# Optimization experiments

Measured on AMD Instinct MI355X. Metric: run time of the kernel, lower is better.

Reference implementation:

```python
import jax, jax.numpy as jnp
import numpy as np

D_MODEL = 1024
N_HEADS = 16
D_HEAD = D_MODEL // N_HEADS


def setup_inputs() -> dict:
    key = jax.random.key(0)
    ks = jax.random.split(key, 9)
    s = 1.0 / np.sqrt(D_MODEL)
    x = jax.random.normal(ks[0], (2, 2048, D_MODEL), dtype=jnp.float32)
    Wq = jax.random.uniform(ks[1], (D_MODEL, D_MODEL), jnp.float32, -s, s)
    bq = jax.random.uniform(ks[2], (D_MODEL,), jnp.float32, -s, s)
    Wk = jax.random.uniform(ks[3], (D_MODEL, D_MODEL), jnp.float32, -s, s)
    bk = jax.random.uniform(ks[4], (D_MODEL,), jnp.float32, -s, s)
    Wv = jax.random.uniform(ks[5], (D_MODEL, D_MODEL), jnp.float32, -s, s)
    bv = jax.random.uniform(ks[6], (D_MODEL,), jnp.float32, -s, s)
    Wo = jax.random.uniform(ks[7], (D_MODEL, D_MODEL), jnp.float32, -s, s)
    bo = jax.random.uniform(ks[8], (D_MODEL,), jnp.float32, -s, s)
    return {"x": x, "Wq": Wq, "bq": bq, "Wk": Wk, "bk": bk,
            "Wv": Wv, "bv": bv, "Wo": Wo, "bo": bo}


def reference(x, Wq, bq, Wk, bk, Wv, bv, Wo, bo):
    B, T, _ = x.shape
    # projections: (B, T, d_model) -> (B, H, T, d_head)
    def split_heads(y):
        return y.reshape(B, T, N_HEADS, D_HEAD).transpose(0, 2, 1, 3)
    Q = split_heads(x @ Wq + bq)
    K = split_heads(x @ Wk + bk)
    V = split_heads(x @ Wv + bv)
    scores = jnp.einsum('bhqd,bhkd->bhqk', Q, K) / jnp.sqrt(jnp.float32(D_HEAD))
    causal = jnp.tril(jnp.ones((T, T), dtype=bool))  # allowed positions
    scores = jnp.where(causal, scores, -jnp.inf)
    attn = jax.nn.softmax(scores, axis=-1)
    out = jnp.einsum('bhqk,bhkd->bhqd', attn, V)
    out = out.transpose(0, 2, 1, 3).reshape(B, T, D_MODEL)
    return out @ Wo + bo
```

## Files before the change

kernel.cpp:

```cpp
#include <hip/hip_runtime.h>

typedef unsigned short u16;
typedef unsigned int u32;

#define DM 1024
#define NH 16
#define DH 64
#define BB 2
#define TT 2048

#define SCLQ 0.18033688f

using frag8  = __attribute__((ext_vector_type(8))) short;
using bf16x8 = __attribute__((ext_vector_type(8))) __bf16;
using f32x4  = __attribute__((ext_vector_type(4))) float;

__device__ inline u16 f2bf(float f) {
  union { float f; u32 u; } v; v.f = f;
  u32 r = v.u + 0x7fffu + ((v.u >> 16) & 1u);
  return (u16)(r >> 16);
}

__device__ inline f32x4 mfma_bf16(frag8 a, frag8 b, f32x4 c) {
  return __builtin_amdgcn_mfma_f32_16x16x32_bf16(
      __builtin_bit_cast(bf16x8, a), __builtin_bit_cast(bf16x8, b), c, 0, 0, 0);
}

__device__ inline void gld16(void* lds, const void* g) {
  __builtin_amdgcn_global_load_lds(
      (const __attribute__((address_space(1))) void*)g,
      (__attribute__((address_space(3))) void*)lds, 16, 0, 0);
}

__device__ inline int swi(int row, int chunk) {
  return row * 64 + ((chunk ^ (row & 7)) << 3);
}

__global__ __launch_bounds__(256) void cvt_x_kernel(const float* __restrict__ X,
                                                    u16* __restrict__ Y) {
  int i = blockIdx.x * 256 + threadIdx.x;
  float4 v = ((const float4*)X)[i];
  ushort4 o;
  o.x = f2bf(v.x); o.y = f2bf(v.y); o.z = f2bf(v.z); o.w = f2bf(v.w);
  ((ushort4*)Y)[i] = o;
}

__global__ __launch_bounds__(256) void transpose_w_kernel(
    const float* __restrict__ W0, const float* __restrict__ W1,
    const float* __restrict__ W2, const float* __restrict__ W3,
    u16* __restrict__ O0, u16* __restrict__ O1,
    u16* __restrict__ O2, u16* __restrict__ O3) {
  const float* W; u16* Ot;
  switch (blockIdx.z) {
    case 0: W = W0; Ot = O0; break;
    case 1: W = W1; Ot = O1; break;
    case 2: W = W2; Ot = O2; break;
    default: W = W3; Ot = O3; break;
  }
  __shared__ u16 Ls[64][72];
  int tid = threadIdx.x;
  int n0 = blockIdx.x * 64;
  int k0 = blockIdx.y * 64;
#pragma unroll
  for (int p = 0; p < 4; ++p) {
    int id = tid + p * 256;
    int row = id >> 4;
    int c4 = (id & 15) * 4;
    float4 v = *(const float4*)&W[(size_t)(k0 + row) * DM + n0 + c4];
    ushort4 o; o.x = f2bf(v.x); o.y = f2bf(v.y); o.z = f2bf(v.z); o.w = f2bf(v.w);
    *(ushort4*)&Ls[row][c4] = o;
  }
  __syncthreads();
#pragma unroll
  for (int p = 0; p < 4; ++p) {
    int id = tid + p * 256;
    int row = id >> 4;
    int c4 = (id & 15) * 4;
    ushort4 o;
    o.x = Ls[c4 + 0][row]; o.y = Ls[c4 + 1][row];
    o.z = Ls[c4 + 2][row]; o.w = Ls[c4 + 3][row];
    *(ushort4*)&Ot[(size_t)(n0 + row) * DM + k0 + c4] = o;
  }
}

__global__ __launch_bounds__(256, 3) void gemm_qkv_kernel(
    const u16* __restrict__ A, const u16* __restrict__ Bt,
    const float* __restrict__ b0, const float* __restrict__ b1,
    const float* __restrict__ b2,
    u16* __restrict__ QK, u16* __restrict__ Vb) {
  constexpr int K = 1024;
  __shared__ u16 As[2][4096];
  __shared__ u16 Bs[2][4096];
  int tid = threadIdx.x;
  int lane = tid & 63, w = tid >> 6;
  int qd = lane >> 4, ln = lane & 15;
  int wm = (w & 1) * 64, wn = (w >> 1) * 64;
  int m0 = blockIdx.y * 128, n0 = blockIdx.x * 128;
  f32x4 z = {0.f, 0.f, 0.f, 0.f};
  f32x4 acc[4][4];
#pragma unroll
  for (int mi = 0; mi < 4; ++mi)
#pragma unroll
    for (int ni = 0; ni < 4; ++ni) acc[mi][ni] = z;

  const u16* ga = A + (size_t)(m0 + w * 32 + (lane >> 2)) * K + (lane & 3) * 8;
  const u16* gb = Bt + (size_t)(n0 + w * 32 + (lane >> 2)) * K + (lane & 3) * 8;

  gld16(&As[0][w * 1024],       ga);
  gld16(&As[0][w * 1024 + 512], ga + 16 * K);
  gld16(&Bs[0][w * 1024],       gb);
  gld16(&Bs[0][w * 1024 + 512], gb + 16 * K);

  for (int k0 = 0; k0 < K; k0 += 32) {
    int cur = (k0 >> 5) & 1;
    __syncthreads();
    if (k0 + 32 < K) {
      int nb = cur ^ 1;
      gld16(&As[nb][w * 1024],       ga + k0 + 32);
      gld16(&As[nb][w * 1024 + 512], ga + k0 + 32 + 16 * K);
      gld16(&Bs[nb][w * 1024],       gb + k0 + 32);
      gld16(&Bs[nb][w * 1024 + 512], gb + k0 + 32 + 16 * K);
    }
    frag8 af[4], bfr[4];
#pragma unroll
    for (int mi = 0; mi < 4; ++mi)
      af[mi] = *(const frag8*)&As[cur][(wm + mi * 16 + ln) * 32 + qd * 8];
#pragma unroll
    for (int ni = 0; ni < 4; ++ni)
      bfr[ni] = *(const frag8*)&Bs[cur][(wn + ni * 16 + ln) * 32 + qd * 8];
#pragma unroll
    for (int mi = 0; mi < 4; ++mi)
#pragma unroll
      for (int ni = 0; ni < 4; ++ni)
        acc[mi][ni] = mfma_bf16(af[mi], bfr[ni], acc[mi][ni]);
  }

#pragma unroll
  for (int ni = 0; ni < 4; ++ni) {
    int col = n0 + wn + ni * 16 + ln;
    if (col < 2048) {
      bool isq = col < 1024;
      float bias = isq ? b0[col] : b1[col - 1024];
#pragma unroll
      for (int mi = 0; mi < 4; ++mi) {
        int row = m0 + wm + mi * 16 + qd * 4;
#pragma unroll
        for (int r = 0; r < 4; ++r) {
          float v = acc[mi][ni][r] + bias;
          if (isq) v *= SCLQ;
          QK[(size_t)(row + r) * 2048 + col] = f2bf(v);
        }
      }
    } else {
      int c2 = col - 2048;
      float bias = b2[c2];
#pragma unroll
      for (int mi = 0; mi < 4; ++mi) {
        int row = m0 + wm + mi * 16 + qd * 4;
#pragma unroll
        for (int r = 0; r < 4; ++r)
          Vb[(size_t)(row + r) * 1024 + c2] = f2bf(acc[mi][ni][r] + bias);
      }
    }
  }
}

__global__ __launch_bounds__(256) void gemm_out_kernel(
    const u16* __restrict__ A, const u16* __restrict__ Bt,
    const float* __restrict__ b0, float* __restrict__ Cf) {
  constexpr int K = 1024;
  __shared__ u16 As[2][4096];
  __shared__ u16 Bs[2][2048];
  int tid = threadIdx.x;
  int lane = tid & 63, w = tid >> 6;
  int qd = lane >> 4, ln = lane & 15;
  int m0 = blockIdx.y * 128, n0 = blockIdx.x * 64;
  f32x4 z = {0.f, 0.f, 0.f, 0.f};
  f32x4 acc[2][4];
#pragma unroll
  for (int mi = 0; mi < 2; ++mi)
#pragma unroll
    for (int ni = 0; ni < 4; ++ni) acc[mi][ni] = z;

  const u16* ga = A + (size_t)(m0 + w * 32 + (lane >> 2)) * K + (lane & 3) * 8;
  const u16* gb = Bt + (size_t)(n0 + w * 16 + (lane >> 2)) * K + (lane & 3) * 8;

  gld16(&As[0][w * 1024],       ga);
  gld16(&As[0][w * 1024 + 512], ga + 16 * K);
  gld16(&Bs[0][w * 512],        gb);

  for (int k0 = 0; k0 < K; k0 += 32) {
    int cur = (k0 >> 5) & 1;
    __syncthreads();
    if (k0 + 32 < K) {
      int nb = cur ^ 1;
      gld16(&As[nb][w * 1024],       ga + k0 + 32);
      gld16(&As[nb][w * 1024 + 512], ga + k0 + 32 + 16 * K);
      gld16(&Bs[nb][w * 512],        gb + k0 + 32);
    }
    frag8 af[2], bfr[4];
#pragma unroll
    for (int mi = 0; mi < 2; ++mi)
      af[mi] = *(const frag8*)&As[cur][(w * 32 + mi * 16 + ln) * 32 + qd * 8];
#pragma unroll
    for (int ni = 0; ni < 4; ++ni)
      bfr[ni] = *(const frag8*)&Bs[cur][(ni * 16 + ln) * 32 + qd * 8];
#pragma unroll
    for (int mi = 0; mi < 2; ++mi)
#pragma unroll
      for (int ni = 0; ni < 4; ++ni)
        acc[mi][ni] = mfma_bf16(af[mi], bfr[ni], acc[mi][ni]);
  }

#pragma unroll
  for (int ni = 0; ni < 4; ++ni) {
    int col = n0 + ni * 16 + ln;
    float bias = b0[col];
#pragma unroll
    for (int mi = 0; mi < 2; ++mi) {
      int row = m0 + w * 32 + mi * 16 + qd * 4;
#pragma unroll
      for (int r = 0; r < 4; ++r)
        Cf[(size_t)(row + r) * 1024 + col] = acc[mi][ni][r] + bias;
    }
  }
}

__global__ __launch_bounds__(256) void transpose_v_kernel(const u16* __restrict__ V,
                                                          u16* __restrict__ Vt) {
  int bh = blockIdx.y;
  int b = bh >> 4, h = bh & 15;
  int t0 = blockIdx.x * 64;
  __shared__ u16 Ls[64][72];
  int tid = threadIdx.x;
#pragma unroll
  for (int p = 0; p < 2; ++p) {
    int id = tid + p * 256;
    int row = id >> 3, seg = id & 7;
    *(uint4*)&Ls[row][seg * 8] =
        *(const uint4*)&V[(size_t)(b * TT + t0 + row) * DM + h * DH + seg * 8];
  }
  __syncthreads();
#pragma unroll
  for (int p = 0; p < 2; ++p) {
    int id = tid + p * 256;
    int d = id >> 3, seg = id & 7;
    union { u16 s[8]; uint4 v; } tmp;
#pragma unroll
    for (int j = 0; j < 8; ++j) tmp.s[j] = Ls[seg * 8 + j][d];
    *(uint4*)&Vt[(size_t)(bh * DH + d) * TT + t0 + seg * 8] = tmp.v;
  }
}

__global__ __launch_bounds__(256, 3) void flash4_kernel(const u16* __restrict__ QK,
                                                        const u16* __restrict__ Vt,
                                                        u16* __restrict__ O) {
  int pj = blockIdx.x;
  int bh = blockIdx.y;
  int b = bh >> 4, h = bh & 15;
  int qtA = pj, qtB = 31 - pj;
  int q0A = qtA * 64, q0B = qtB * 64;
  __shared__ u16 Ks[2 * 4096];
  __shared__ u16 Vs[2 * 4096];
  __shared__ u16 PsA[4096];
  __shared__ u16 PsB[4096];
  int tid = threadIdx.x;
  int lane = tid & 63, w = tid >> 6;
  int qd = lane >> 4, ln = lane & 15;

  frag8 qfA[2], qfB[2];
#pragma unroll
  for (int kk = 0; kk < 2; ++kk) {
    qfA[kk] = *(const frag8*)&QK[(size_t)(b * TT + q0A + w * 16 + ln) * 2048 +
                                 h * 64 + kk * 32 + qd * 8];
    qfB[kk] = *(const frag8*)&QK[(size_t)(b * TT + q0B + w * 16 + ln) * 2048 +
                                 h * 64 + kk * 32 + qd * 8];
  }

  int lr = lane >> 3, lc = (lane & 7) ^ lr;
  const u16* KgA = &QK[(size_t)(b * TT + w * 16 + lr) * 2048 + 1024 + h * 64 + lc * 8];
  const u16* KgB = KgA + 8 * 2048;
  const u16* VgA = &Vt[(size_t)(bh * 64 + w * 16 + lr) * 2048 + lc * 8];
  const u16* VgB = VgA + 8 * 2048;
  int ldsw = w * 1024;

  int nkt = qtB + 1;

  gld16(&Ks[ldsw],       KgA);
  gld16(&Ks[ldsw + 512], KgB);
  gld16(&Vs[ldsw],       VgA);
  gld16(&Vs[ldsw + 512], VgB);

  float lA = 0.f, lB = 0.f;
  f32x4 z = {0.f, 0.f, 0.f, 0.f};
  f32x4 oA[4] = {z, z, z, z};
  f32x4 oB[4] = {z, z, z, z};

  for (int kt = 0; kt < nkt; ++kt) {
    int cur = kt & 1;
    int cb = cur * 4096;
    __syncthreads();

    if (kt + 1 < nkt) {
      int nb = (cur ^ 1) * 4096;
      size_t ko = (size_t)(kt + 1) * 64 * 2048;
      int vo = (kt + 1) * 64;
      gld16(&Ks[nb + ldsw],       KgA + ko);
      gld16(&Ks[nb + ldsw + 512], KgB + ko);
      gld16(&Vs[nb + ldsw],       VgA + vo);
      gld16(&Vs[nb + ldsw + 512], VgB + vo);
    }

    bool actA  = (kt <= qtA);
    bool diagA = (kt == qtA);
    bool diagB = (kt == qtB);

    f32x4 sA[4] = {z, z, z, z};
    f32x4 sB[4] = {z, z, z, z};
#pragma unroll
    for (int mi = 0; mi < 4; ++mi) {
      bool skipB = diagB && (mi > w);
      bool doA = actA && !(diagA && (mi > w));
      if (skipB && !doA) continue;
#pragma unroll
      for (int kk = 0; kk < 2; ++kk) {
        frag8 ak = *(const frag8*)&Ks[cb + swi(mi * 16 + ln, 4 * kk + qd)];
        if (!skipB) sB[mi] = mfma_bf16(ak, qfB[kk], sB[mi]);
        if (doA)    sA[mi] = mfma_bf16(ak, qfA[kk], sA[mi]);
      }
    }

    auto softmax_store = [&](f32x4* s, bool diag, u16* Ps, float& lacc) {
#pragma unroll
      for (int mi = 0; mi < 4; ++mi) {
        int pb = swi(w * 16 + ln, 2 * mi + (qd >> 1)) + (qd & 1) * 4;
        if (diag && mi > w) {
          uint2 zz; zz.x = 0u; zz.y = 0u;
          *(uint2*)&Ps[pb] = zz;
          continue;
        }
        float p0 = __builtin_amdgcn_exp2f(s[mi][0]);
        float p1 = __builtin_amdgcn_exp2f(s[mi][1]);
        float p2 = __builtin_amdgcn_exp2f(s[mi][2]);
        float p3 = __builtin_amdgcn_exp2f(s[mi][3]);
        if (diag && mi == w) {
          p0 = (qd * 4 + 0 <= ln) ? p0 : 0.f;
          p1 = (qd * 4 + 1 <= ln) ? p1 : 0.f;
          p2 = (qd * 4 + 2 <= ln) ? p2 : 0.f;
          p3 = (qd * 4 + 3 <= ln) ? p3 : 0.f;
        }
        lacc += (p0 + p1) + (p2 + p3);
        u32 u0 = __builtin_bit_cast(u32, p0) + 0x8000u;
        u32 u1 = __builtin_bit_cast(u32, p1) + 0x8000u;
        u32 u2 = __builtin_bit_cast(u32, p2) + 0x8000u;
        u32 u3 = __builtin_bit_cast(u32, p3) + 0x8000u;
        uint2 pk;
        pk.x = __builtin_amdgcn_perm(u1, u0, 0x07060302u);
        pk.y = __builtin_amdgcn_perm(u3, u2, 0x07060302u);
        *(uint2*)&Ps[pb] = pk;
      }
    };
    softmax_store(sB, diagB, PsB, lB);
    if (actA) softmax_store(sA, diagA, PsA, lA);

#pragma unroll
    for (int kk = 0; kk < 2; ++kk) {
      if (diagB && kk == 1 && w < 2) continue;
      frag8 bpB = *(const frag8*)&PsB[swi(w * 16 + ln, 4 * kk + qd)];
      frag8 bpA;
      if (actA) bpA = *(const frag8*)&PsA[swi(w * 16 + ln, 4 * kk + qd)];
#pragma unroll
      for (int mi = 0; mi < 4; ++mi) {
        frag8 av = *(const frag8*)&Vs[cb + swi(mi * 16 + ln, 4 * kk + qd)];
        oB[mi] = mfma_bf16(av, bpB, oB[mi]);
        if (actA) oA[mi] = mfma_bf16(av, bpA, oA[mi]);
      }
    }
  }

  lA += __shfl_xor(lA, 16); lA += __shfl_xor(lA, 32);
  lB += __shfl_xor(lB, 16); lB += __shfl_xor(lB, 32);
  float rlA = 1.0f / lA, rlB = 1.0f / lB;

#pragma unroll
  for (int mi = 0; mi < 4; ++mi) {
    ushort4 ov;
    ov.x = f2bf(oA[mi][0] * rlA); ov.y = f2bf(oA[mi][1] * rlA);
    ov.z = f2bf(oA[mi][2] * rlA); ov.w = f2bf(oA[mi][3] * rlA);
    *(ushort4*)&O[(size_t)(b * TT + q0A + w * 16 + ln) * DM + h * 64 + mi * 16 + qd * 4] = ov;
    ov.x = f2bf(oB[mi][0] * rlB); ov.y = f2bf(oB[mi][1] * rlB);
    ov.z = f2bf(oB[mi][2] * rlB); ov.w = f2bf(oB[mi][3] * rlB);
    *(ushort4*)&O[(size_t)(b * TT + q0B + w * 16 + ln) * DM + h * 64 + mi * 16 + qd * 4] = ov;
  }
}

extern "C" void kernel_launch(void* const* d_in, const int* in_sizes, int n_in,
                              void* d_out, int out_size, void* d_ws, size_t ws_size,
                              hipStream_t stream) {
  const float* x  = (const float*)d_in[0];
  const float* Wq = (const float*)d_in[1];
  const float* bq = (const float*)d_in[2];
  const float* Wk = (const float*)d_in[3];
  const float* bk = (const float*)d_in[4];
  const float* Wv = (const float*)d_in[5];
  const float* bv = (const float*)d_in[6];
  const float* Wo = (const float*)d_in[7];
  const float* bo = (const float*)d_in[8];

  char* ws = (char*)d_ws;
  const size_t MB = 1ull << 20;
  u16* xbf  = (u16*)(ws + 0);
  u16* Wcat = (u16*)(ws + 8 * MB);
  u16* Wot  = (u16*)(ws + 14 * MB);
  u16* QKb  = (u16*)(ws + 16 * MB);
  u16* Vbb  = (u16*)(ws + 32 * MB);
  u16* Vtb  = (u16*)(ws + 40 * MB);
  u16* Ob   = (u16*)(ws + 48 * MB);

  cvt_x_kernel<<<4096, 256, 0, stream>>>(x, xbf);
  transpose_w_kernel<<<dim3(16, 16, 4), 256, 0, stream>>>(
      Wq, Wk, Wv, Wo, Wcat, Wcat + 1024 * 1024, Wcat + 2 * 1024 * 1024, Wot);
  gemm_qkv_kernel<<<dim3(24, 32), 256, 0, stream>>>(
      xbf, Wcat, bq, bk, bv, QKb, Vbb);
  transpose_v_kernel<<<dim3(32, 32), 256, 0, stream>>>(Vbb, Vtb);
  flash4_kernel<<<dim3(16, 32), 256, 0, stream>>>(QKb, Vtb, Ob);
  gemm_out_kernel<<<dim3(16, 32), 256, 0, stream>>>(Ob, Wot, bo, (float*)d_out);
}
```

Before: 212.3 us.

## Swizzle GEMM LDS tiles and restructure flash kernel to single tile with bpermute P

```diff
diff --git a/kernel.cpp b/kernel.cpp
--- a/kernel.cpp
+++ b/kernel.cpp
@@ -103,14 +103,16 @@
 #pragma unroll
     for (int ni = 0; ni < 4; ++ni) acc[mi][ni] = z;
 
-  const u16* ga = A + (size_t)(m0 + w * 32 + (lane >> 2)) * K + (lane & 3) * 8;
-  const u16* gb = Bt + (size_t)(n0 + w * 32 + (lane >> 2)) * K + (lane & 3) * 8;
+  int csw = ((lane & 3) ^ ((lane >> 2) & 3)) * 8;
+  const u16* ga = A + (size_t)(m0 + w * 32 + (lane >> 2)) * K + csw;
+  const u16* gb = Bt + (size_t)(n0 + w * 32 + (lane >> 2)) * K + csw;
 
   gld16(&As[0][w * 1024],       ga);
   gld16(&As[0][w * 1024 + 512], ga + 16 * K);
   gld16(&Bs[0][w * 1024],       gb);
   gld16(&Bs[0][w * 1024 + 512], gb + 16 * K);
 
+  int fsw = (qd ^ (ln & 3)) * 8;
   for (int k0 = 0; k0 < K; k0 += 32) {
     int cur = (k0 >> 5) & 1;
     __syncthreads();
@@ -124,10 +126,10 @@
     frag8 af[4], bfr[4];
 #pragma unroll
     for (int mi = 0; mi < 4; ++mi)
-      af[mi] = *(const frag8*)&As[cur][(wm + mi * 16 + ln) * 32 + qd * 8];
+      af[mi] = *(const frag8*)&As[cur][(wm + mi * 16 + ln) * 32 + fsw];
 #pragma unroll
     for (int ni = 0; ni < 4; ++ni)
-      bfr[ni] = *(const frag8*)&Bs[cur][(wn + ni * 16 + ln) * 32 + qd * 8];
+      bfr[ni] = *(const frag8*)&Bs[cur][(wn + ni * 16 + ln) * 32 + fsw];
 #pragma unroll
     for (int mi = 0; mi < 4; ++mi)
 #pragma unroll
@@ -182,13 +184,15 @@
 #pragma unroll
     for (int ni = 0; ni < 4; ++ni) acc[mi][ni] = z;
 
-  const u16* ga = A + (size_t)(m0 + w * 32 + (lane >> 2)) * K + (lane & 3) * 8;
-  const u16* gb = Bt + (size_t)(n0 + w * 16 + (lane >> 2)) * K + (lane & 3) * 8;
+  int csw = ((lane & 3) ^ ((lane >> 2) & 3)) * 8;
+  const u16* ga = A + (size_t)(m0 + w * 32 + (lane >> 2)) * K + csw;
+  const u16* gb = Bt + (size_t)(n0 + w * 16 + (lane >> 2)) * K + csw;
 
   gld16(&As[0][w * 1024],       ga);
   gld16(&As[0][w * 1024 + 512], ga + 16 * K);
   gld16(&Bs[0][w * 512],        gb);
 
+  int fsw = (qd ^ (ln & 3)) * 8;
   for (int k0 = 0; k0 < K; k0 += 32) {
     int cur = (k0 >> 5) & 1;
     __syncthreads();
@@ -201,10 +205,10 @@
     frag8 af[2], bfr[4];
 #pragma unroll
     for (int mi = 0; mi < 2; ++mi)
-      af[mi] = *(const frag8*)&As[cur][(w * 32 + mi * 16 + ln) * 32 + qd * 8];
+      af[mi] = *(const frag8*)&As[cur][(w * 32 + mi * 16 + ln) * 32 + fsw];
 #pragma unroll
     for (int ni = 0; ni < 4; ++ni)
-      bfr[ni] = *(const frag8*)&Bs[cur][(ni * 16 + ln) * 32 + qd * 8];
+      bfr[ni] = *(const frag8*)&Bs[cur][(ni * 16 + ln) * 32 + fsw];
 #pragma unroll
     for (int mi = 0; mi < 2; ++mi)
 #pragma unroll
@@ -252,30 +256,24 @@
   }
 }
 
-__global__ __launch_bounds__(256, 3) void flash4_kernel(const u16* __restrict__ QK,
+__global__ __launch_bounds__(256, 4) void flash5_kernel(const u16* __restrict__ QK,
                                                         const u16* __restrict__ Vt,
                                                         u16* __restrict__ O) {
-  int pj = blockIdx.x;
+  int qt = 31 - (int)blockIdx.x;
   int bh = blockIdx.y;
   int b = bh >> 4, h = bh & 15;
-  int qtA = pj, qtB = 31 - pj;
-  int q0A = qtA * 64, q0B = qtB * 64;
+  int q0 = qt * 64;
   __shared__ u16 Ks[2 * 4096];
   __shared__ u16 Vs[2 * 4096];
-  __shared__ u16 PsA[4096];
-  __shared__ u16 PsB[4096];
   int tid = threadIdx.x;
   int lane = tid & 63, w = tid >> 6;
   int qd = lane >> 4, ln = lane & 15;
 
-  frag8 qfA[2], qfB[2];
-#pragma unroll
-  for (int kk = 0; kk < 2; ++kk) {
-    qfA[kk] = *(const frag8*)&QK[(size_t)(b * TT + q0A + w * 16 + ln) * 2048 +
-                                 h * 64 + kk * 32 + qd * 8];
-    qfB[kk] = *(const frag8*)&QK[(size_t)(b * TT + q0B + w * 16 + ln) * 2048 +
-                                 h * 64 + kk * 32 + qd * 8];
-  }
+  frag8 qf[2];
+#pragma unroll
+  for (int kk = 0; kk < 2; ++kk)
+    qf[kk] = *(const frag8*)&QK[(size_t)(b * TT + q0 + w * 16 + ln) * 2048 +
+                                h * 64 + kk * 32 + qd * 8];
 
   int lr = lane >> 3, lc = (lane & 7) ^ lr;
   const u16* KgA = &QK[(size_t)(b * TT + w * 16 + lr) * 2048 + 1024 + h * 64 + lc * 8];
@@ -284,17 +282,18 @@
   const u16* VgB = VgA + 8 * 2048;
   int ldsw = w * 1024;
 
-  int nkt = qtB + 1;
-
+  int idxg0 = ((((2 * qd) & 3) * 16 + ln) * 4);
+  int idxg1 = ((((2 * qd + 1) & 3) * 16 + ln) * 4);
+
+  int nkt = qt + 1;
   gld16(&Ks[ldsw],       KgA);
   gld16(&Ks[ldsw + 512], KgB);
   gld16(&Vs[ldsw],       VgA);
   gld16(&Vs[ldsw + 512], VgB);
 
-  float lA = 0.f, lB = 0.f;
+  float l_part = 0.f;
   f32x4 z = {0.f, 0.f, 0.f, 0.f};
-  f32x4 oA[4] = {z, z, z, z};
-  f32x4 oB[4] = {z, z, z, z};
+  f32x4 o_acc[4] = {z, z, z, z};
 
   for (int kt = 0; kt < nkt; ++kt) {
     int cur = kt & 1;
@@ -311,86 +310,80 @@
       gld16(&Vs[nb + ldsw + 512], VgB + vo);
     }
 
-    bool actA  = (kt <= qtA);
-    bool diagA = (kt == qtA);
-    bool diagB = (kt == qtB);
-
-    f32x4 sA[4] = {z, z, z, z};
-    f32x4 sB[4] = {z, z, z, z};
+    bool diag = (kt == qt);
+
+    f32x4 s[4] = {z, z, z, z};
 #pragma unroll
     for (int mi = 0; mi < 4; ++mi) {
-      bool skipB = diagB && (mi > w);
-      bool doA = actA && !(diagA && (mi > w));
-      if (skipB && !doA) continue;
+      if (diag && mi > w) continue;
 #pragma unroll
       for (int kk = 0; kk < 2; ++kk) {
         frag8 ak = *(const frag8*)&Ks[cb + swi(mi * 16 + ln, 4 * kk + qd)];
-        if (!skipB) sB[mi] = mfma_bf16(ak, qfB[kk], sB[mi]);
-        if (doA)    sA[mi] = mfma_bf16(ak, qfA[kk], sA[mi]);
+        s[mi] = mfma_bf16(ak, qf[kk], s[mi]);
       }
     }
 
-    auto softmax_store = [&](f32x4* s, bool diag, u16* Ps, float& lacc) {
-#pragma unroll
-      for (int mi = 0; mi < 4; ++mi) {
-        int pb = swi(w * 16 + ln, 2 * mi + (qd >> 1)) + (qd & 1) * 4;
-        if (diag && mi > w) {
-          uint2 zz; zz.x = 0u; zz.y = 0u;
-          *(uint2*)&Ps[pb] = zz;
-          continue;
-        }
-        float p0 = __builtin_amdgcn_exp2f(s[mi][0]);
-        float p1 = __builtin_amdgcn_exp2f(s[mi][1]);
-        float p2 = __builtin_amdgcn_exp2f(s[mi][2]);
-        float p3 = __builtin_amdgcn_exp2f(s[mi][3]);
-        if (diag && mi == w) {
-          p0 = (qd * 4 + 0 <= ln) ? p0 : 0.f;
-          p1 = (qd * 4 + 1 <= ln) ? p1 : 0.f;
-          p2 = (qd * 4 + 2 <= ln) ? p2 : 0.f;
-          p3 = (qd * 4 + 3 <= ln) ? p3 : 0.f;
-        }
-        lacc += (p0 + p1) + (p2 + p3);
-        u32 u0 = __builtin_bit_cast(u32, p0) + 0x8000u;
-        u32 u1 = __builtin_bit_cast(u32, p1) + 0x8000u;
-        u32 u2 = __builtin_bit_cast(u32, p2) + 0x8000u;
-        u32 u3 = __builtin_bit_cast(u32, p3) + 0x8000u;
-        uint2 pk;
-        pk.x = __builtin_amdgcn_perm(u1, u0, 0x07060302u);
-        pk.y = __builtin_amdgcn_perm(u3, u2, 0x07060302u);
-        *(uint2*)&Ps[pb] = pk;
+    u32 pk[4][2];
+#pragma unroll
+    for (int mi = 0; mi < 4; ++mi) {
+      if (diag && mi > w) { pk[mi][0] = 0u; pk[mi][1] = 0u; continue; }
+      float p0 = __builtin_amdgcn_exp2f(s[mi][0]);
+      float p1 = __builtin_amdgcn_exp2f(s[mi][1]);
+      float p2 = __builtin_amdgcn_exp2f(s[mi][2]);
+      float p3 = __builtin_amdgcn_exp2f(s[mi][3]);
+      if (diag && mi == w) {
+        p0 = (qd * 4 + 0 <= ln) ? p0 : 0.f;
+        p1 = (qd * 4 + 1 <= ln) ? p1 : 0.f;
+        p2 = (qd * 4 + 2 <= ln) ? p2 : 0.f;
+        p3 = (qd * 4 + 3 <= ln) ? p3 : 0.f;
       }
-    };
-    softmax_store(sB, diagB, PsB, lB);
-    if (actA) softmax_store(sA, diagA, PsA, lA);
+      l_part += (p0 + p1) + (p2 + p3);
+      u32 u0 = __builtin_bit_cast(u32, p0) + 0x8000u;
+      u32 u1 = __builtin_bit_cast(u32, p1) + 0x8000u;
+      u32 u2 = __builtin_bit_cast(u32, p2) + 0x8000u;
+      u32 u3 = __builtin_bit_cast(u32, p3) + 0x8000u;
+      pk[mi][0] = __builtin_amdgcn_perm(u1, u0, 0x07060302u);
+      pk[mi][1] = __builtin_amdgcn_perm(u3, u2, 0x07060302u);
+    }
 
 #pragma unroll
     for (int kk = 0; kk < 2; ++kk) {
-      if (diagB && kk == 1 && w < 2) continue;
-      frag8 bpB = *(const frag8*)&PsB[swi(w * 16 + ln, 4 * kk + qd)];
-      frag8 bpA;
-      if (actA) bpA = *(const frag8*)&PsA[swi(w * 16 + ln, 4 * kk + qd)];
+      if (diag && kk == 1 && w < 2) continue;
+      u32 a0 = __builtin_amdgcn_ds_bpermute(idxg0, (int)pk[2 * kk][0]);
+      u32 a1 = __builtin_amdgcn_ds_bpermute(idxg0, (int)pk[2 * kk][1]);
+      u32 a2 = __builtin_amdgcn_ds_bpermute(idxg1, (int)pk[2 * kk][0]);
+      u32 a3 = __builtin_amdgcn_ds_bpermute(idxg1, (int)pk[2 * kk][1]);
+      u32 c0 = __builtin_amdgcn_ds_bpermute(idxg0, (int)pk[2 * kk + 1][0]);
+      u32 c1 = __builtin_amdgcn_ds_bpermute(idxg0, (int)pk[2 * kk + 1][1]);
+      u32 c2 = __builtin_amdgcn_ds_bpermute(idxg1, (int)pk[2 * kk + 1][0]);
+      u32 c3 = __builtin_amdgcn_ds_bpermute(idxg1, (int)pk[2 * kk + 1][1]);
+      bool hi = qd >= 2;
+      uint4 bpv;
+      bpv.x = hi ? c0 : a0;
+      bpv.y = hi ? c1 : a1;
+      bpv.z = hi ? c2 : a2;
+      bpv.w = hi ? c3 : a3;
+      frag8 bp = __builtin_bit_cast(frag8, bpv);
 #pragma unroll
       for (int mi = 0; mi < 4; ++mi) {
         frag8 av = *(const frag8*)&Vs[cb + swi(mi * 16 + ln, 4 * kk + qd)];
-        oB[mi] = mfma_bf16(av, bpB, oB[mi]);
-        if (actA) oA[mi] = mfma_bf16(av, bpA, oA[mi]);
+        o_acc[mi] = mfma_bf16(av, bp, o_acc[mi]);
       }
     }
   }
 
-  lA += __shfl_xor(lA, 16); lA += __shfl_xor(lA, 32);
-  lB += __shfl_xor(lB, 16); lB += __shfl_xor(lB, 32);
-  float rlA = 1.0f / lA, rlB = 1.0f / lB;
+  l_part += __shfl_xor(l_part, 16);
+  l_part += __shfl_xor(l_part, 32);
+  float rl = 1.0f / l_part;
 
 #pragma unroll
   for (int mi = 0; mi < 4; ++mi) {
     ushort4 ov;
-    ov.x = f2bf(oA[mi][0] * rlA); ov.y = f2bf(oA[mi][1] * rlA);
-    ov.z = f2bf(oA[mi][2] * rlA); ov.w = f2bf(oA[mi][3] * rlA);
-    *(ushort4*)&O[(size_t)(b * TT + q0A + w * 16 + ln) * DM + h * 64 + mi * 16 + qd * 4] = ov;
-    ov.x = f2bf(oB[mi][0] * rlB); ov.y = f2bf(oB[mi][1] * rlB);
-    ov.z = f2bf(oB[mi][2] * rlB); ov.w = f2bf(oB[mi][3] * rlB);
-    *(ushort4*)&O[(size_t)(b * TT + q0B + w * 16 + ln) * DM + h * 64 + mi * 16 + qd * 4] = ov;
+    ov.x = f2bf(o_acc[mi][0] * rl);
+    ov.y = f2bf(o_acc[mi][1] * rl);
+    ov.z = f2bf(o_acc[mi][2] * rl);
+    ov.w = f2bf(o_acc[mi][3] * rl);
+    *(ushort4*)&O[(size_t)(b * TT + q0 + w * 16 + ln) * DM + h * 64 + mi * 16 + qd * 4] = ov;
   }
 }
 
@@ -423,6 +416,6 @@
   gemm_qkv_kernel<<<dim3(24, 32), 256, 0, stream>>>(
       xbf, Wcat, bq, bk, bv, QKb, Vbb);
   transpose_v_kernel<<<dim3(32, 32), 256, 0, stream>>>(Vbb, Vtb);
-  flash4_kernel<<<dim3(16, 32), 256, 0, stream>>>(QKb, Vtb, Ob);
+  flash5_kernel<<<dim3(32, 32), 256, 0, stream>>>(QKb, Vtb, Ob);
   gemm_out_kernel<<<dim3(16, 32), 256, 0, stream>>>(Ob, Wot, bo, (float*)d_out);
 }
```

Measured after the change: 225.5 us. +6.2%, slower.

## Keep softmax probabilities in registers for PV MFMA and swizzle GEMM LDS tiles

Applied to the files above, without the earlier changes.

```diff
diff --git a/kernel.cpp b/kernel.cpp
--- a/kernel.cpp
+++ b/kernel.cpp
@@ -12,6 +12,7 @@
 #define SCLQ 0.18033688f
 
 using frag8  = __attribute__((ext_vector_type(8))) short;
+using frag4  = __attribute__((ext_vector_type(4))) short;
 using bf16x8 = __attribute__((ext_vector_type(8))) __bf16;
 using f32x4  = __attribute__((ext_vector_type(4))) float;
 
@@ -26,6 +27,10 @@
       __builtin_bit_cast(bf16x8, a), __builtin_bit_cast(bf16x8, b), c, 0, 0, 0);
 }
 
+__device__ inline f32x4 mfma16_bf16(frag4 a, frag4 b, f32x4 c) {
+  return __builtin_amdgcn_mfma_f32_16x16x16bf16_1k(a, b, c, 0, 0, 0);
+}
+
 __device__ inline void gld16(void* lds, const void* g) {
   __builtin_amdgcn_global_load_lds(
       (const __attribute__((address_space(1))) void*)g,
@@ -34,6 +39,10 @@
 
 __device__ inline int swi(int row, int chunk) {
   return row * 64 + ((chunk ^ (row & 7)) << 3);
+}
+__device__ inline int vswi(int row, int kq, int qd) {
+  int c = 2 * kq + (qd >> 1);
+  return row * 64 + ((c ^ (row & 7)) << 3) + ((qd & 1) << 2);
 }
 
 __global__ __launch_bounds__(256) void cvt_x_kernel(const float* __restrict__ X,
@@ -103,14 +112,16 @@
 #pragma unroll
     for (int ni = 0; ni < 4; ++ni) acc[mi][ni] = z;
 
-  const u16* ga = A + (size_t)(m0 + w * 32 + (lane >> 2)) * K + (lane & 3) * 8;
-  const u16* gb = Bt + (size_t)(n0 + w * 32 + (lane >> 2)) * K + (lane & 3) * 8;
+  int csw = ((lane & 3) ^ ((lane >> 2) & 3)) * 8;
+  const u16* ga = A + (size_t)(m0 + w * 32 + (lane >> 2)) * K + csw;
+  const u16* gb = Bt + (size_t)(n0 + w * 32 + (lane >> 2)) * K + csw;
 
   gld16(&As[0][w * 1024],       ga);
   gld16(&As[0][w * 1024 + 512], ga + 16 * K);
   gld16(&Bs[0][w * 1024],       gb);
   gld16(&Bs[0][w * 1024 + 512], gb + 16 * K);
 
+  int fsw = (qd ^ (ln & 3)) * 8;
   for (int k0 = 0; k0 < K; k0 += 32) {
     int cur = (k0 >> 5) & 1;
     __syncthreads();
@@ -124,10 +135,10 @@
     frag8 af[4], bfr[4];
 #pragma unroll
     for (int mi = 0; mi < 4; ++mi)
-      af[mi] = *(const frag8*)&As[cur][(wm + mi * 16 + ln) * 32 + qd * 8];
+      af[mi] = *(const frag8*)&As[cur][(wm + mi * 16 + ln) * 32 + fsw];
 #pragma unroll
     for (int ni = 0; ni < 4; ++ni)
-      bfr[ni] = *(const frag8*)&Bs[cur][(wn + ni * 16 + ln) * 32 + qd * 8];
+      bfr[ni] = *(const frag8*)&Bs[cur][(wn + ni * 16 + ln) * 32 + fsw];
 #pragma unroll
     for (int mi = 0; mi < 4; ++mi)
 #pragma unroll
@@ -182,13 +193,15 @@
 #pragma unroll
     for (int ni = 0; ni < 4; ++ni) acc[mi][ni] = z;
 
-  const u16* ga = A + (size_t)(m0 + w * 32 + (lane >> 2)) * K + (lane & 3) * 8;
-  const u16* gb = Bt + (size_t)(n0 + w * 16 + (lane >> 2)) * K + (lane & 3) * 8;
+  int csw = ((lane & 3) ^ ((lane >> 2) & 3)) * 8;
+  const u16* ga = A + (size_t)(m0 + w * 32 + (lane >> 2)) * K + csw;
+  const u16* gb = Bt + (size_t)(n0 + w * 16 + (lane >> 2)) * K + csw;
 
   gld16(&As[0][w * 1024],       ga);
   gld16(&As[0][w * 1024 + 512], ga + 16 * K);
   gld16(&Bs[0][w * 512],        gb);
 
+  int fsw = (qd ^ (ln & 3)) * 8;
   for (int k0 = 0; k0 < K; k0 += 32) {
     int cur = (k0 >> 5) & 1;
     __syncthreads();
@@ -201,10 +214,10 @@
     frag8 af[2], bfr[4];
 #pragma unroll
     for (int mi = 0; mi < 2; ++mi)
-      af[mi] = *(const frag8*)&As[cur][(w * 32 + mi * 16 + ln) * 32 + qd * 8];
+      af[mi] = *(const frag8*)&As[cur][(w * 32 + mi * 16 + ln) * 32 + fsw];
 #pragma unroll
     for (int ni = 0; ni < 4; ++ni)
-      bfr[ni] = *(const frag8*)&Bs[cur][(ni * 16 + ln) * 32 + qd * 8];
+      bfr[ni] = *(const frag8*)&Bs[cur][(ni * 16 + ln) * 32 + fsw];
 #pragma unroll
     for (int mi = 0; mi < 2; ++mi)
 #pragma unroll
@@ -252,7 +265,7 @@
   }
 }
 
-__global__ __launch_bounds__(256, 3) void flash4_kernel(const u16* __restrict__ QK,
+__global__ __launch_bounds__(256, 4) void flash6_kernel(const u16* __restrict__ QK,
                                                         const u16* __restrict__ Vt,
                                                         u16* __restrict__ O) {
   int pj = blockIdx.x;
@@ -262,8 +275,6 @@
   int q0A = qtA * 64, q0B = qtB * 64;
   __shared__ u16 Ks[2 * 4096];
   __shared__ u16 Vs[2 * 4096];
-  __shared__ u16 PsA[4096];
-  __shared__ u16 PsB[4096];
   int tid = threadIdx.x;
   int lane = tid & 63, w = tid >> 6;
   int qd = lane >> 4, ln = lane & 15;
@@ -285,7 +296,6 @@
   int ldsw = w * 1024;
 
   int nkt = qtB + 1;
-
   gld16(&Ks[ldsw],       KgA);
   gld16(&Ks[ldsw + 512], KgB);
   gld16(&Vs[ldsw],       VgA);
@@ -330,15 +340,11 @@
       }
     }
 
-    auto softmax_store = [&](f32x4* s, bool diag, u16* Ps, float& lacc) {
+    u32 pkA[4][2], pkB[4][2];
+    auto softmax_pack = [&](f32x4* s, bool diag, u32 (*pk)[2], float& lacc) {
 #pragma unroll
       for (int mi = 0; mi < 4; ++mi) {
-        int pb = swi(w * 16 + ln, 2 * mi + (qd >> 1)) + (qd & 1) * 4;
-        if (diag && mi > w) {
-          uint2 zz; zz.x = 0u; zz.y = 0u;
-          *(uint2*)&Ps[pb] = zz;
-          continue;
-        }
+        if (diag && mi > w) { pk[mi][0] = 0u; pk[mi][1] = 0u; continue; }
         float p0 = __builtin_amdgcn_exp2f(s[mi][0]);
         float p1 = __builtin_amdgcn_exp2f(s[mi][1]);
         float p2 = __builtin_amdgcn_exp2f(s[mi][2]);
@@ -354,26 +360,28 @@
         u32 u1 = __builtin_bit_cast(u32, p1) + 0x8000u;
         u32 u2 = __builtin_bit_cast(u32, p2) + 0x8000u;
         u32 u3 = __builtin_bit_cast(u32, p3) + 0x8000u;
-        uint2 pk;
-        pk.x = __builtin_amdgcn_perm(u1, u0, 0x07060302u);
-        pk.y = __builtin_amdgcn_perm(u3, u2, 0x07060302u);
-        *(uint2*)&Ps[pb] = pk;
+        pk[mi][0] = __builtin_amdgcn_perm(u1, u0, 0x07060302u);
+        pk[mi][1] = __builtin_amdgcn_perm(u3, u2, 0x07060302u);
       }
     };
-    softmax_store(sB, diagB, PsB, lB);
-    if (actA) softmax_store(sA, diagA, PsA, lA);
-
-#pragma unroll
-    for (int kk = 0; kk < 2; ++kk) {
-      if (diagB && kk == 1 && w < 2) continue;
-      frag8 bpB = *(const frag8*)&PsB[swi(w * 16 + ln, 4 * kk + qd)];
-      frag8 bpA;
-      if (actA) bpA = *(const frag8*)&PsA[swi(w * 16 + ln, 4 * kk + qd)];
-#pragma unroll
-      for (int mi = 0; mi < 4; ++mi) {
-        frag8 av = *(const frag8*)&Vs[cb + swi(mi * 16 + ln, 4 * kk + qd)];
-        oB[mi] = mfma_bf16(av, bpB, oB[mi]);
-        if (actA) oA[mi] = mfma_bf16(av, bpA, oA[mi]);
+    softmax_pack(sB, diagB, pkB, lB);
+    if (actA) softmax_pack(sA, diagA, pkA, lA);
+
+#pragma unroll
+    for (int kq = 0; kq < 4; ++kq) {
+      bool skipB = diagB && (kq > w);
+      bool doA = actA && !(diagA && (kq > w));
+      if (skipB && !doA) continue;
+      uint2 tb; tb.x = pkB[kq][0]; tb.y = pkB[kq][1];
+      frag4 bpB = __builtin_bit_cast(frag4, tb);
+      frag4 bpA;
+      if (doA) { uint2 ta; ta.x = pkA[kq][0]; ta.y = pkA[kq][1];
+                 bpA = __builtin_bit_cast(frag4, ta); }
+#pragma unroll
+      for (int di = 0; di < 4; ++di) {
+        frag4 av = *(const frag4*)&Vs[cb + vswi(di * 16 + ln, kq, qd)];
+        if (!skipB) oB[di] = mfma16_bf16(av, bpB, oB[di]);
+        if (doA)    oA[di] = mfma16_bf16(av, bpA, oA[di]);
       }
     }
   }
@@ -383,14 +391,14 @@
   float rlA = 1.0f / lA, rlB = 1.0f / lB;
 
 #pragma unroll
-  for (int mi = 0; mi < 4; ++mi) {
+  for (int di = 0; di < 4; ++di) {
     ushort4 ov;
-    ov.x = f2bf(oA[mi][0] * rlA); ov.y = f2bf(oA[mi][1] * rlA);
-    ov.z = f2bf(oA[mi][2] * rlA); ov.w = f2bf(oA[mi][3] * rlA);
-    *(ushort4*)&O[(size_t)(b * TT + q0A + w * 16 + ln) * DM + h * 64 + mi * 16 + qd * 4] = ov;
-    ov.x = f2bf(oB[mi][0] * rlB); ov.y = f2bf(oB[mi][1] * rlB);
-    ov.z = f2bf(oB[mi][2] * rlB); ov.w = f2bf(oB[mi][3] * rlB);
-    *(ushort4*)&O[(size_t)(b * TT + q0B + w * 16 + ln) * DM + h * 64 + mi * 16 + qd * 4] = ov;
+    ov.x = f2bf(oA[di][0] * rlA); ov.y = f2bf(oA[di][1] * rlA);
+    ov.z = f2bf(oA[di][2] * rlA); ov.w = f2bf(oA[di][3] * rlA);
+    *(ushort4*)&O[(size_t)(b * TT + q0A + w * 16 + ln) * DM + h * 64 + di * 16 + qd * 4] = ov;
+    ov.x = f2bf(oB[di][0] * rlB); ov.y = f2bf(oB[di][1] * rlB);
+    ov.z = f2bf(oB[di][2] * rlB); ov.w = f2bf(oB[di][3] * rlB);
+    *(ushort4*)&O[(size_t)(b * TT + q0B + w * 16 + ln) * DM + h * 64 + di * 16 + qd * 4] = ov;
   }
 }
 
@@ -423,6 +431,6 @@
   gemm_qkv_kernel<<<dim3(24, 32), 256, 0, stream>>>(
       xbf, Wcat, bq, bk, bv, QKb, Vbb);
   transpose_v_kernel<<<dim3(32, 32), 256, 0, stream>>>(Vbb, Vtb);
-  flash4_kernel<<<dim3(16, 32), 256, 0, stream>>>(QKb, Vtb, Ob);
+  flash6_kernel<<<dim3(16, 32), 256, 0, stream>>>(QKb, Vtb, Ob);
   gemm_out_kernel<<<dim3(16, 32), 256, 0, stream>>>(Ob, Wot, bo, (float*)d_out);
 }
```

New measurement: 220.4 us. 1.04x slower.

## Software-pipeline flash attention with triple-buffered K/V and swizzle GEMM LDS tiles

Applied to the files above, without the earlier changes.

```diff
diff --git a/kernel.cpp b/kernel.cpp
--- a/kernel.cpp
+++ b/kernel.cpp
@@ -103,14 +103,16 @@
 #pragma unroll
     for (int ni = 0; ni < 4; ++ni) acc[mi][ni] = z;
 
-  const u16* ga = A + (size_t)(m0 + w * 32 + (lane >> 2)) * K + (lane & 3) * 8;
-  const u16* gb = Bt + (size_t)(n0 + w * 32 + (lane >> 2)) * K + (lane & 3) * 8;
+  int csw = ((lane & 3) ^ ((lane >> 2) & 3)) * 8;
+  const u16* ga = A + (size_t)(m0 + w * 32 + (lane >> 2)) * K + csw;
+  const u16* gb = Bt + (size_t)(n0 + w * 32 + (lane >> 2)) * K + csw;
 
   gld16(&As[0][w * 1024],       ga);
   gld16(&As[0][w * 1024 + 512], ga + 16 * K);
   gld16(&Bs[0][w * 1024],       gb);
   gld16(&Bs[0][w * 1024 + 512], gb + 16 * K);
 
+  int fsw = (qd ^ (ln & 3)) * 8;
   for (int k0 = 0; k0 < K; k0 += 32) {
     int cur = (k0 >> 5) & 1;
     __syncthreads();
@@ -124,10 +126,10 @@
     frag8 af[4], bfr[4];
 #pragma unroll
     for (int mi = 0; mi < 4; ++mi)
-      af[mi] = *(const frag8*)&As[cur][(wm + mi * 16 + ln) * 32 + qd * 8];
+      af[mi] = *(const frag8*)&As[cur][(wm + mi * 16 + ln) * 32 + fsw];
 #pragma unroll
     for (int ni = 0; ni < 4; ++ni)
-      bfr[ni] = *(const frag8*)&Bs[cur][(wn + ni * 16 + ln) * 32 + qd * 8];
+      bfr[ni] = *(const frag8*)&Bs[cur][(wn + ni * 16 + ln) * 32 + fsw];
 #pragma unroll
     for (int mi = 0; mi < 4; ++mi)
 #pragma unroll
@@ -182,13 +184,15 @@
 #pragma unroll
     for (int ni = 0; ni < 4; ++ni) acc[mi][ni] = z;
 
-  const u16* ga = A + (size_t)(m0 + w * 32 + (lane >> 2)) * K + (lane & 3) * 8;
-  const u16* gb = Bt + (size_t)(n0 + w * 16 + (lane >> 2)) * K + (lane & 3) * 8;
+  int csw = ((lane & 3) ^ ((lane >> 2) & 3)) * 8;
+  const u16* ga = A + (size_t)(m0 + w * 32 + (lane >> 2)) * K + csw;
+  const u16* gb = Bt + (size_t)(n0 + w * 16 + (lane >> 2)) * K + csw;
 
   gld16(&As[0][w * 1024],       ga);
   gld16(&As[0][w * 1024 + 512], ga + 16 * K);
   gld16(&Bs[0][w * 512],        gb);
 
+  int fsw = (qd ^ (ln & 3)) * 8;
   for (int k0 = 0; k0 < K; k0 += 32) {
     int cur = (k0 >> 5) & 1;
     __syncthreads();
@@ -201,10 +205,10 @@
     frag8 af[2], bfr[4];
 #pragma unroll
     for (int mi = 0; mi < 2; ++mi)
-      af[mi] = *(const frag8*)&As[cur][(w * 32 + mi * 16 + ln) * 32 + qd * 8];
+      af[mi] = *(const frag8*)&As[cur][(w * 32 + mi * 16 + ln) * 32 + fsw];
 #pragma unroll
     for (int ni = 0; ni < 4; ++ni)
-      bfr[ni] = *(const frag8*)&Bs[cur][(ni * 16 + ln) * 32 + qd * 8];
+      bfr[ni] = *(const frag8*)&Bs[cur][(ni * 16 + ln) * 32 + fsw];
 #pragma unroll
     for (int mi = 0; mi < 2; ++mi)
 #pragma unroll
@@ -252,7 +256,7 @@
   }
 }
 
-__global__ __launch_bounds__(256, 3) void flash4_kernel(const u16* __restrict__ QK,
+__global__ __launch_bounds__(256, 2) void flash7_kernel(const u16* __restrict__ QK,
                                                         const u16* __restrict__ Vt,
                                                         u16* __restrict__ O) {
   int pj = blockIdx.x;
@@ -260,8 +264,8 @@
   int b = bh >> 4, h = bh & 15;
   int qtA = pj, qtB = 31 - pj;
   int q0A = qtA * 64, q0B = qtB * 64;
-  __shared__ u16 Ks[2 * 4096];
-  __shared__ u16 Vs[2 * 4096];
+  __shared__ u16 Ks[3 * 4096];
+  __shared__ u16 Vs[3 * 4096];
   __shared__ u16 PsA[4096];
   __shared__ u16 PsB[4096];
   int tid = threadIdx.x;
@@ -286,41 +290,18 @@
 
   int nkt = qtB + 1;
 
-  gld16(&Ks[ldsw],       KgA);
-  gld16(&Ks[ldsw + 512], KgB);
-  gld16(&Vs[ldsw],       VgA);
-  gld16(&Vs[ldsw + 512], VgB);
-
   float lA = 0.f, lB = 0.f;
   f32x4 z = {0.f, 0.f, 0.f, 0.f};
   f32x4 oA[4] = {z, z, z, z};
   f32x4 oB[4] = {z, z, z, z};
 
-  for (int kt = 0; kt < nkt; ++kt) {
-    int cur = kt & 1;
-    int cb = cur * 4096;
-    __syncthreads();
-
-    if (kt + 1 < nkt) {
-      int nb = (cur ^ 1) * 4096;
-      size_t ko = (size_t)(kt + 1) * 64 * 2048;
-      int vo = (kt + 1) * 64;
-      gld16(&Ks[nb + ldsw],       KgA + ko);
-      gld16(&Ks[nb + ldsw + 512], KgB + ko);
-      gld16(&Vs[nb + ldsw],       VgA + vo);
-      gld16(&Vs[nb + ldsw + 512], VgB + vo);
-    }
-
-    bool actA  = (kt <= qtA);
-    bool diagA = (kt == qtA);
-    bool diagB = (kt == qtB);
-
-    f32x4 sA[4] = {z, z, z, z};
-    f32x4 sB[4] = {z, z, z, z};
+  auto compute_S = [&](int j, int slot, f32x4* sA, f32x4* sB) {
+    int cb = slot * 4096;
+    bool actA_ = (j <= qtA), diagA_ = (j == qtA), diagB_ = (j == qtB);
 #pragma unroll
     for (int mi = 0; mi < 4; ++mi) {
-      bool skipB = diagB && (mi > w);
-      bool doA = actA && !(diagA && (mi > w));
+      bool skipB = diagB_ && (mi > w);
+      bool doA = actA_ && !(diagA_ && (mi > w));
       if (skipB && !doA) continue;
 #pragma unroll
       for (int kk = 0; kk < 2; ++kk) {
@@ -329,53 +310,104 @@
         if (doA)    sA[mi] = mfma_bf16(ak, qfA[kk], sA[mi]);
       }
     }
-
-    auto softmax_store = [&](f32x4* s, bool diag, u16* Ps, float& lacc) {
-#pragma unroll
-      for (int mi = 0; mi < 4; ++mi) {
-        int pb = swi(w * 16 + ln, 2 * mi + (qd >> 1)) + (qd & 1) * 4;
-        if (diag && mi > w) {
-          uint2 zz; zz.x = 0u; zz.y = 0u;
-          *(uint2*)&Ps[pb] = zz;
-          continue;
+  };
+
+  auto softmax_store = [&](f32x4* s, bool act, bool diag, u16* Ps, float& lacc) {
+    if (!act) return;
+#pragma unroll
+    for (int mi = 0; mi < 4; ++mi) {
+      int pb = swi(w * 16 + ln, 2 * mi + (qd >> 1)) + (qd & 1) * 4;
+      if (diag && mi > w) {
+        uint2 zz; zz.x = 0u; zz.y = 0u;
+        *(uint2*)&Ps[pb] = zz;
+        continue;
+      }
+      float p0 = __builtin_amdgcn_exp2f(s[mi][0]);
+      float p1 = __builtin_amdgcn_exp2f(s[mi][1]);
+      float p2 = __builtin_amdgcn_exp2f(s[mi][2]);
+      float p3 = __builtin_amdgcn_exp2f(s[mi][3]);
+      if (diag && mi == w) {
+        p0 = (qd * 4 + 0 <= ln) ? p0 : 0.f;
+        p1 = (qd * 4 + 1 <= ln) ? p1 : 0.f;
+        p2 = (qd * 4 + 2 <= ln) ? p2 : 0.f;
+        p3 = (qd * 4 + 3 <= ln) ? p3 : 0.f;
+      }
+      lacc += (p0 + p1) + (p2 + p3);
+      u32 u0 = __builtin_bit_cast(u32, p0) + 0x8000u;
+      u32 u1 = __builtin_bit_cast(u32, p1) + 0x8000u;
+      u32 u2 = __builtin_bit_cast(u32, p2) + 0x8000u;
+      u32 u3 = __builtin_bit_cast(u32, p3) + 0x8000u;
+      uint2 pk;
+      pk.x = __builtin_amdgcn_perm(u1, u0, 0x07060302u);
+      pk.y = __builtin_amdgcn_perm(u3, u2, 0x07060302u);
+      *(uint2*)&Ps[pb] = pk;
+    }
+  };
+
+  gld16(&Ks[ldsw],            KgA);
+  gld16(&Ks[ldsw + 512],      KgB);
+  gld16(&Vs[ldsw],            VgA);
+  gld16(&Vs[ldsw + 512],      VgB);
+  {
+    size_t ko = (size_t)64 * 2048;
+    gld16(&Ks[4096 + ldsw],       KgA + ko);
+    gld16(&Ks[4096 + ldsw + 512], KgB + ko);
+    gld16(&Vs[4096 + ldsw],       VgA + 64);
+    gld16(&Vs[4096 + ldsw + 512], VgB + 64);
+  }
+  __syncthreads();
+
+  {
+    f32x4 sA[4] = {z, z, z, z};
+    f32x4 sB[4] = {z, z, z, z};
+    compute_S(0, 0, sA, sB);
+    softmax_store(sA, true, qtA == 0, PsA, lA);
+    softmax_store(sB, true, false, PsB, lB);
+  }
+
+  for (int kt = 0; kt < nkt; ++kt) {
+    if (kt + 2 < nkt) {
+      int ns = ((kt + 2) % 3) * 4096;
+      size_t ko = (size_t)(kt + 2) * 64 * 2048;
+      int vo = (kt + 2) * 64;
+      gld16(&Ks[ns + ldsw],       KgA + ko);
+      gld16(&Ks[ns + ldsw + 512], KgB + ko);
+      gld16(&Vs[ns + ldsw],       VgA + vo);
+      gld16(&Vs[ns + ldsw + 512], VgB + vo);
+    }
+
+    int j = kt + 1;
+    bool hasNext = (j < nkt);
+
+    f32x4 sA[4] = {z, z, z, z};
+    f32x4 sB[4] = {z, z, z, z};
+    if (hasNext) compute_S(j, j % 3, sA, sB);
+
+    {
+      int cb = (kt % 3) * 4096;
+      bool diagB_pv = (kt == qtB);
+      bool actA_pv = (kt <= qtA);
+#pragma unroll
+      for (int kk = 0; kk < 2; ++kk) {
+        if (diagB_pv && kk == 1 && w < 2) continue;
+        frag8 bpB = *(const frag8*)&PsB[swi(w * 16 + ln, 4 * kk + qd)];
+        frag8 bpA;
+        if (actA_pv) bpA = *(const frag8*)&PsA[swi(w * 16 + ln, 4 * kk + qd)];
+#pragma unroll
+        for (int mi = 0; mi < 4; ++mi) {
+          frag8 av = *(const frag8*)&Vs[cb + swi(mi * 16 + ln, 4 * kk + qd)];
+          oB[mi] = mfma_bf16(av, bpB, oB[mi]);
+          if (actA_pv) oA[mi] = mfma_bf16(av, bpA, oA[mi]);
         }
-        float p0 = __builtin_amdgcn_exp2f(s[mi][0]);
-        float p1 = __builtin_amdgcn_exp2f(s[mi][1]);
-        float p2 = __builtin_amdgcn_exp2f(s[mi][2]);
-        float p3 = __builtin_amdgcn_exp2f(s[mi][3]);
-        if (diag && mi == w) {
-          p0 = (qd * 4 + 0 <= ln) ? p0 : 0.f;
-          p1 = (qd * 4 + 1 <= ln) ? p1 : 0.f;
-          p2 = (qd * 4 + 2 <= ln) ? p2 : 0.f;
-          p3 = (qd * 4 + 3 <= ln) ? p3 : 0.f;
-        }
-        lacc += (p0 + p1) + (p2 + p3);
-        u32 u0 = __builtin_bit_cast(u32, p0) + 0x8000u;
-        u32 u1 = __builtin_bit_cast(u32, p1) + 0x8000u;
-        u32 u2 = __builtin_bit_cast(u32, p2) + 0x8000u;
-        u32 u3 = __builtin_bit_cast(u32, p3) + 0x8000u;
-        uint2 pk;
-        pk.x = __builtin_amdgcn_perm(u1, u0, 0x07060302u);
-        pk.y = __builtin_amdgcn_perm(u3, u2, 0x07060302u);
-        *(uint2*)&Ps[pb] = pk;
-      }
-    };
-    softmax_store(sB, diagB, PsB, lB);
-    if (actA) softmax_store(sA, diagA, PsA, lA);
-
-#pragma unroll
-    for (int kk = 0; kk < 2; ++kk) {
-      if (diagB && kk == 1 && w < 2) continue;
-      frag8 bpB = *(const frag8*)&PsB[swi(w * 16 + ln, 4 * kk + qd)];
-      frag8 bpA;
-      if (actA) bpA = *(const frag8*)&PsA[swi(w * 16 + ln, 4 * kk + qd)];
-#pragma unroll
-      for (int mi = 0; mi < 4; ++mi) {
-        frag8 av = *(const frag8*)&Vs[cb + swi(mi * 16 + ln, 4 * kk + qd)];
-        oB[mi] = mfma_bf16(av, bpB, oB[mi]);
-        if (actA) oA[mi] = mfma_bf16(av, bpA, oA[mi]);
-      }
-    }
+      }
+    }
+
+    if (hasNext) {
+      softmax_store(sA, j <= qtA, j == qtA, PsA, lA);
+      softmax_store(sB, true, j == qtB, PsB, lB);
+    }
+
+    __syncthreads();
   }
 
   lA += __shfl_xor(lA, 16); lA += __shfl_xor(lA, 32);
@@ -383,14 +415,14 @@
   float rlA = 1.0f / lA, rlB = 1.0f / lB;
 
 #pragma unroll
-  for (int mi = 0; mi < 4; ++mi) {
+  for (int di = 0; di < 4; ++di) {
     ushort4 ov;
-    ov.x = f2bf(oA[mi][0] * rlA); ov.y = f2bf(oA[mi][1] * rlA);
-    ov.z = f2bf(oA[mi][2] * rlA); ov.w = f2bf(oA[mi][3] * rlA);
-    *(ushort4*)&O[(size_t)(b * TT + q0A + w * 16 + ln) * DM + h * 64 + mi * 16 + qd * 4] = ov;
-    ov.x = f2bf(oB[mi][0] * rlB); ov.y = f2bf(oB[mi][1] * rlB);
-    ov.z = f2bf(oB[mi][2] * rlB); ov.w = f2bf(oB[mi][3] * rlB);
-    *(ushort4*)&O[(size_t)(b * TT + q0B + w * 16 + ln) * DM + h * 64 + mi * 16 + qd * 4] = ov;
+    ov.x = f2bf(oA[di][0] * rlA); ov.y = f2bf(oA[di][1] * rlA);
+    ov.z = f2bf(oA[di][2] * rlA); ov.w = f2bf(oA[di][3] * rlA);
+    *(ushort4*)&O[(size_t)(b * TT + q0A + w * 16 + ln) * DM + h * 64 + di * 16 + qd * 4] = ov;
+    ov.x = f2bf(oB[di][0] * rlB); ov.y = f2bf(oB[di][1] * rlB);
+    ov.z = f2bf(oB[di][2] * rlB); ov.w = f2bf(oB[di][3] * rlB);
+    *(ushort4*)&O[(size_t)(b * TT + q0B + w * 16 + ln) * DM + h * 64 + di * 16 + qd * 4] = ov;
   }
 }
 
@@ -423,6 +455,6 @@
   gemm_qkv_kernel<<<dim3(24, 32), 256, 0, stream>>>(
       xbf, Wcat, bq, bk, bv, QKb, Vbb);
   transpose_v_kernel<<<dim3(32, 32), 256, 0, stream>>>(Vbb, Vtb);
-  flash4_kernel<<<dim3(16, 32), 256, 0, stream>>>(QKb, Vtb, Ob);
+  flash7_kernel<<<dim3(16, 32), 256, 0, stream>>>(QKb, Vtb, Ob);
   gemm_out_kernel<<<dim3(16, 32), 256, 0, stream>>>(Ob, Wot, bo, (float*)d_out);
 }
```

Measured after the change: 218.1 us. +2.7%, slower.
